# Kernel tuning notes

Hardware: AMD Instinct MI355X
Metric: run time of the kernel (lower is better)

The kernel has to match this reference:

```python
import jax, jax.numpy as jnp
import numpy as np
from jax import lax

D = 1024          # d_model
ORDER = 2         # hyena order
FILT = 64         # filter_order (implicit MLP width)
EMB = 3           # positional embedding dim (default)
INNER = D * (ORDER + 1)
DF = D * (ORDER - 1)   # filter d_model
L_MAX = 2048


def setup_inputs() -> dict:
    key = jax.random.key(0)
    ks = jax.random.split(key, 16)
    s = 0.02
    return {
        "u": jax.random.normal(ks[0], (4, L_MAX, D), jnp.float32),
        "in_w": jax.random.normal(ks[1], (D, INNER), jnp.float32) * s,
        "in_b": jnp.zeros((INNER,), jnp.float32),
        "short_w": jax.random.normal(ks[2], (INNER, 3), jnp.float32) * 0.3,
        "short_b": jnp.zeros((INNER,), jnp.float32),
        "mlp_w1": jax.random.normal(ks[3], (EMB, FILT), jnp.float32) * 0.3,
        "mlp_b1": jnp.zeros((FILT,), jnp.float32),
        "mlp_w2": jax.random.normal(ks[4], (FILT, FILT), jnp.float32) * 0.1,
        "mlp_b2": jnp.zeros((FILT,), jnp.float32),
        "mlp_w3": jax.random.normal(ks[5], (FILT, FILT), jnp.float32) * 0.1,
        "mlp_b3": jnp.zeros((FILT,), jnp.float32),
        "mlp_wo": jax.random.normal(ks[6], (FILT, DF), jnp.float32) * 0.1,
        "freq": jnp.ones((1, FILT), jnp.float32),       # shared Sin freq (w=1)
        "filt_bias": jax.random.normal(ks[7], (DF,), jnp.float32),
        "out_w": jax.random.normal(ks[8], (D, D), jnp.float32) * s,
        "out_b": jnp.zeros((D,), jnp.float32),
    }


def _pos_emb(L):
    # PositionalEmbedding(emb_dim=3): t, real/imag of exp(-i f w), bands=(3-1)//2=1
    t = jnp.linspace(0.0, 1.0, L)[:, None]                      # (L,1)
    tr = jnp.linspace(0.0, L - 1.0, L)[:, None]
    w = 2.0 * np.pi * tr / L                                    # (L,1)
    f = jnp.array([1e-4], jnp.float32)[None, :]                  # bands=1
    z = jnp.concatenate([t, jnp.cos(f * w), -jnp.sin(f * w)], axis=-1)  # (L,3)
    return z, t


def _decay(t):
    # ExponentialModulation: target=1e-2, fast=0.3, slow=1.5, shift=0
    max_d = np.log(1e-2) / 0.3
    min_d = np.log(1e-2) / 1.5
    deltas = jnp.linspace(min_d, max_d, DF)[None, :]             # (1,DF)
    return jnp.exp(-t * jnp.abs(deltas))                         # (L,DF)


def reference(u, in_w, in_b, short_w, short_b, mlp_w1, mlp_b1, mlp_w2, mlp_b2,
              mlp_w3, mlp_b3, mlp_wo, freq, filt_bias, out_w, out_b):
    B, L, _ = u.shape
    # in_proj: b l d -> b l (3d) -> b (3d) l
    up = jnp.einsum('bld,de->ble', u, in_w) + in_b
    up = up.transpose(0, 2, 1)                                   # (B, INNER, L)
    # depthwise short conv, kernel 3, padding 2 both sides, then [:L]
    uc = lax.conv_general_dilated(up, short_w[:, None, :], (1,), [(2, 2)],
                                  feature_group_count=INNER,
                                  dimension_numbers=('NCH', 'OIH', 'NCH'))
    uc = uc[..., :L] + short_b[None, :, None]
    x0, x1, v = uc[:, :D], uc[:, D:2 * D], uc[:, 2 * D:]
    # implicit long filter k(L): pos-emb -> Sin MLP (shared freq) -> modulation
    z, t = _pos_emb(L)
    h = jnp.sin(freq * (z @ mlp_w1 + mlp_b1))
    h = jnp.sin(freq * (h @ mlp_w2 + mlp_b2))
    h = jnp.sin(freq * (h @ mlp_w3 + mlp_b3))
    h = h @ mlp_wo                                               # (L, DF)
    k = (h * _decay(t)).T                                        # (DF, L) == (D, L) for order=2
    # hyena recurrence: order-1 = 1 gated fft-conv step
    vx = v * x1                                                  # (B, D, L)
    n = 2 * L
    y = jnp.fft.irfft(jnp.fft.rfft(vx, n=n) * jnp.fft.rfft(k, n=n), n=n)[..., :L]
    v = y + vx * filt_bias[None, :, None]
    # final gate + out_proj
    yv = (v * x0).transpose(0, 2, 1)                             # (B, L, D)
    return jnp.einsum('bld,de->ble', yv, out_w) + out_b
```

## Files before the change

### kernel.cpp

```cpp
#include <hip/hip_runtime.h>
#include <math.h>

#define M_PIf 3.14159265358979323846f
#define MIND (-3.0701134573253936f)
#define MAXD (-15.350567286626968f)

typedef __attribute__((ext_vector_type(8))) _Float16 f16x8;
typedef __attribute__((ext_vector_type(4))) float f32x4;
typedef __attribute__((ext_vector_type(8))) unsigned short u16x8;

#define GLDS(g, l) __builtin_amdgcn_global_load_lds(                         \
    (const __attribute__((address_space(1))) void*)(g),                      \
    (__attribute__((address_space(3))) void*)(l), 16, 0, 0)

__device__ __forceinline__ unsigned short f2h(float x) {
    return __builtin_bit_cast(unsigned short, (_Float16)x);
}
__device__ __forceinline__ float h2f(unsigned short h) {
    return (float)__builtin_bit_cast(_Float16, h);
}

__global__ __launch_bounds__(256) void prep_kernel(
    const float* __restrict__ u, unsigned short* __restrict__ uh,
    const float* __restrict__ in_w, unsigned short* __restrict__ w1t,
    const float* __restrict__ w1, const float* __restrict__ b1,
    const float* __restrict__ w2, const float* __restrict__ b2,
    const float* __restrict__ w3, const float* __restrict__ b3,
    const float* __restrict__ wo, const float* __restrict__ freq,
    float* __restrict__ kbuf)
{
    __shared__ char sm[4352];
    const int bid = blockIdx.x;
    const int tid = threadIdx.x;

    if (bid < 8192) {
        const int i = bid * 256 + tid;
        float4 v = ((const float4*)u)[i];
        ushort4 h;
        h.x = f2h(v.x); h.y = f2h(v.y); h.z = f2h(v.z); h.w = f2h(v.w);
        ((ushort4*)uh)[i] = h;
    } else if (bid < 11264) {
        float (*t)[33] = (float(*)[33])sm;
        const int idx = bid - 8192;
        const int bx = idx % 96, by = idx / 96;
        const int r0 = by * 32, c0 = bx * 32;
        const int tx = tid & 31, ty = tid >> 5;
#pragma unroll
        for (int q = 0; q < 4; ++q) {
            int r = ty + q * 8;
            t[r][tx] = in_w[(size_t)(r0 + r) * 3072 + c0 + tx];
        }
        __syncthreads();
#pragma unroll
        for (int q = 0; q < 4; ++q) {
            int cc = ty + q * 8;
            w1t[(size_t)(c0 + cc) * 1024 + r0 + tx] = f2h(t[tx][cc]);
        }
    } else {
        float (*ha)[65] = (float(*)[65])sm;
        float (*hb)[65] = (float(*)[65])(sm + 2080);
        const int l0 = (bid - 11264) * 8;
        const int uu = tid & 63, lq = tid >> 6;
#pragma unroll
        for (int p = 0; p < 2; ++p) {
            int ll = lq + p * 4;
            int l = l0 + ll;
            float t = (float)l * (1.0f / 2047.0f);
            float ang = 1e-4f * (2.0f * M_PIf) * ((float)l / 2048.0f);
            float pre = t * w1[uu] + cosf(ang) * w1[64 + uu] - sinf(ang) * w1[128 + uu] + b1[uu];
            ha[ll][uu] = sinf(freq[uu] * pre);
        }
        __syncthreads();
#pragma unroll
        for (int p = 0; p < 2; ++p) {
            int ll = lq + p * 4;
            float s = b2[uu];
#pragma unroll
            for (int i = 0; i < 64; ++i) s += ha[ll][i] * w2[i * 64 + uu];
            hb[ll][uu] = sinf(freq[uu] * s);
        }
        __syncthreads();
#pragma unroll
        for (int p = 0; p < 2; ++p) {
            int ll = lq + p * 4;
            float s = b3[uu];
#pragma unroll
            for (int i = 0; i < 64; ++i) s += hb[ll][i] * w3[i * 64 + uu];
            ha[ll][uu] = sinf(freq[uu] * s);
        }
        __syncthreads();

        float acc[4][8] = {};
        for (int i = 0; i < 64; ++i) {
            float wv[4];
#pragma unroll
            for (int q = 0; q < 4; ++q) wv[q] = wo[i * 1024 + tid + 256 * q];
#pragma unroll
            for (int l = 0; l < 8; ++l) {
                float hv = ha[l][i];
#pragma unroll
                for (int q = 0; q < 4; ++q) acc[q][l] += hv * wv[q];
            }
        }
        const float span = (MAXD - MIND) * (1.0f / 1023.0f);
#pragma unroll
        for (int q = 0; q < 4; ++q) {
            int dd = tid + 256 * q;
            float ad = fabsf(MIND + span * (float)dd);
#pragma unroll
            for (int l = 0; l < 8; ++l) {
                float t = (float)(l0 + l) * (1.0f / 2047.0f);
                kbuf[(size_t)dd * 2048 + l0 + l] = acc[q][l] * expf(-t * ad);
            }
        }
    }
}

__global__ __launch_bounds__(256) void post_kernel(
    const unsigned short* __restrict__ yvh, unsigned short* __restrict__ yvt,
    const float* __restrict__ out_w, unsigned short* __restrict__ w2t)
{
    __shared__ char sm[8448];
    const int bid = blockIdx.x;
    const int tid = threadIdx.x;
    if (bid < 2048) {
        unsigned short (*t)[66] = (unsigned short(*)[66])sm;
        const int l0 = (bid & 31) * 64;
        const int d0 = ((bid >> 5) & 15) * 64;
        const int b  = bid >> 9;
        const int rr = tid >> 4, cc = (tid & 15) * 4;
#pragma unroll
        for (int p = 0; p < 4; ++p) {
            int r = p * 16 + rr;
            ushort4 v = *(const ushort4*)&yvh[((size_t)b * 1024 + d0 + r) * 2048 + l0 + cc];
            t[cc + 0][r] = v.x; t[cc + 1][r] = v.y; t[cc + 2][r] = v.z; t[cc + 3][r] = v.w;
        }
        __syncthreads();
#pragma unroll
        for (int p = 0; p < 4; ++p) {
            int r = p * 16 + rr;
            ushort4 o;
            o.x = t[r][cc + 0]; o.y = t[r][cc + 1]; o.z = t[r][cc + 2]; o.w = t[r][cc + 3];
            *(ushort4*)&yvt[((size_t)b * 2048 + l0 + r) * 1024 + d0 + cc] = o;
        }
    } else {
        float (*t)[33] = (float(*)[33])sm;
        const int idx = bid - 2048;
        const int bx = idx & 31, by = idx >> 5;
        const int r0 = by * 32, c0 = bx * 32;
        const int tx = tid & 31, ty = tid >> 5;
#pragma unroll
        for (int q = 0; q < 4; ++q) {
            int r = ty + q * 8;
            t[r][tx] = out_w[(size_t)(r0 + r) * 1024 + c0 + tx];
        }
        __syncthreads();
#pragma unroll
        for (int q = 0; q < 4; ++q) {
            int cc = ty + q * 8;
            w2t[(size_t)(c0 + cc) * 1024 + r0 + tx] = f2h(t[tx][cc]);
        }
    }
}

template <int TRANS_OUT>
__global__ __launch_bounds__(512, 1) void gemm8_f16_kernel(
    const unsigned short* __restrict__ A, const unsigned short* __restrict__ B,
    const float* __restrict__ bias, void* __restrict__ outp)
{
    __shared__ char smem[98304];
    const int tid = threadIdx.x;
    const int wave = tid >> 6, lane = tid & 63;
    const int n0 = blockIdx.x * 128, m0 = blockIdx.y * 256;
    const int wm = wave >> 1, wn = wave & 1;
    const int rr = lane & 15, g4 = lane >> 4;
    const int srow4 = lane >> 2;
    const int sswz  = ((lane & 3) ^ ((lane >> 3) & 3)) * 8;
    const int axor  = (g4 ^ ((rr >> 1) & 3)) * 16;

    f32x4 acc[4][4] = {};
    f16x8 bq[4];

    auto stageA = [&](int bufo, int t, int kh) {
        const int ke = t * 64 + kh * 32;
        char* ldsb = smem + bufo + kh * 16384 + wave * 1024;
#pragma unroll
        for (int j = 0; j < 2; ++j) {
            const int rg = j * 128 + wave * 16 + srow4;
            GLDS((const char*)(A + (size_t)(m0 + rg) * 1024 + ke + sswz), ldsb + j * 8192);
        }
    };
    auto stageB = [&](int bufo, int t, int kh) {
        const int ke = t * 64 + kh * 32;
        const int rg = wave * 16 + srow4;
        GLDS((const char*)(B + (size_t)(n0 + rg) * 1024 + ke + sswz),
             smem + bufo + 32768 + kh * 8192 + wave * 1024);
    };

    auto phase = [&](int bufo, int s, int h, auto stage_fn, int vm) {
        const char* bb = smem + bufo;
        f16x8 aq0, aq1;
        if (h == 0) {
#pragma unroll
            for (int j = 0; j < 4; ++j)
                bq[j] = *(const f16x8*)(bb + 32768 + s * 8192 + (wn * 64 + j * 16 + rr) * 64 + axor);
        }
        aq0 = *(const f16x8*)(bb + s * 16384 + (wm * 64 + (h * 2 + 0) * 16 + rr) * 64 + axor);
        aq1 = *(const f16x8*)(bb + s * 16384 + (wm * 64 + (h * 2 + 1) * 16 + rr) * 64 + axor);
        stage_fn();
        __builtin_amdgcn_s_barrier();
        __builtin_amdgcn_s_setprio(1);
#pragma unroll
        for (int j = 0; j < 4; ++j)
            acc[h * 2 + 0][j] = __builtin_amdgcn_mfma_f32_16x16x32_f16(aq0, bq[j], acc[h * 2 + 0][j], 0, 0, 0);
#pragma unroll
        for (int j = 0; j < 4; ++j)
            acc[h * 2 + 1][j] = __builtin_amdgcn_mfma_f32_16x16x32_f16(aq1, bq[j], acc[h * 2 + 1][j], 0, 0, 0);
        __builtin_amdgcn_s_setprio(0);
        if (vm == 1) asm volatile("s_waitcnt vmcnt(3)" ::: "memory");
        else if (vm == 2) asm volatile("s_waitcnt vmcnt(0)" ::: "memory");
        __builtin_amdgcn_s_barrier();
    };

    stageA(0, 0, 0); stageB(0, 0, 0);
    stageA(0, 0, 1); stageB(0, 0, 1);
    stageA(49152, 1, 0); stageB(49152, 1, 0);
    asm volatile("s_waitcnt vmcnt(0)" ::: "memory");
    __syncthreads();

    for (int it = 0; it < 8; ++it) {
        const int T1 = 2 * it + 1, T2 = 2 * it + 2, T3 = 2 * it + 3;
        const int vmL = (it == 7) ? 2 : 1;
        phase(0,     0, 0, [&] { stageA(49152, T1, 1); }, 0);
        phase(0,     0, 1, [&] { stageB(49152, T1, 1); }, 0);
        phase(0,     1, 0, [&] { if (T2 < 16) stageA(0, T2, 0); }, 0);
        phase(0,     1, 1, [&] { if (T2 < 16) stageB(0, T2, 0); }, vmL);
        phase(49152, 0, 0, [&] { if (T2 < 16) stageA(0, T2, 1); }, 0);
        phase(49152, 0, 1, [&] { if (T2 < 16) stageB(0, T2, 1); }, 0);
        phase(49152, 1, 0, [&] { if (T3 < 16) stageA(49152, T3, 0); }, 0);
        phase(49152, 1, 1, [&] { if (T3 < 16) stageB(49152, T3, 0); }, vmL);
    }

    const int c = rr;
    if (TRANS_OUT) {
        unsigned short* up = (unsigned short*)outp;
        const int bidx = m0 >> 11;
        const int lbase = (m0 & 2047) + wm * 64 + g4 * 4;
#pragma unroll
        for (int j = 0; j < 4; ++j) {
            const int e = n0 + wn * 64 + j * 16 + c;
            const float bv = bias[e];
            unsigned short* dst = up + ((size_t)bidx * 3072 + e) * 2048 + lbase;
#pragma unroll
            for (int i = 0; i < 4; ++i) {
                ushort4 o;
                o.x = f2h(acc[i][j][0] + bv);
                o.y = f2h(acc[i][j][1] + bv);
                o.z = f2h(acc[i][j][2] + bv);
                o.w = f2h(acc[i][j][3] + bv);
                *(ushort4*)(dst + i * 16) = o;
            }
        }
    } else {
        float* op = (float*)outp;
#pragma unroll
        for (int j = 0; j < 4; ++j) {
            const int col = n0 + wn * 64 + j * 16 + c;
            const float bv = bias[col];
#pragma unroll
            for (int i = 0; i < 4; ++i) {
                const int row = m0 + wm * 64 + i * 16 + g4 * 4;
#pragma unroll
                for (int r = 0; r < 4; ++r)
                    op[(size_t)(row + r) * 1024 + col] = acc[i][j][r] + bv;
            }
        }
    }
}

__device__ __forceinline__ void conv3_chunk(
    const unsigned short* __restrict__ row, int l0,
    float wa, float wb, float wc, float sbv, float out[8])
{
    f16x8 m = *(const f16x8*)(row + l0);
    float e[10];
    if (l0 > 0) {
        ushort2 p = *(const ushort2*)(row + l0 - 2);
        e[0] = h2f(p.x); e[1] = h2f(p.y);
    } else {
        e[0] = 0.f; e[1] = 0.f;
    }
#pragma unroll
    for (int i = 0; i < 8; ++i) e[2 + i] = (float)m[i];
#pragma unroll
    for (int i = 0; i < 8; ++i)
        out[i] = wa * e[i] + wb * e[i + 1] + wc * e[i + 2] + sbv;
}

__global__ __launch_bounds__(256, 4) void conv_kernel(
    const unsigned short* __restrict__ up_t, const float* __restrict__ kbuf,
    const float* __restrict__ sw, const float* __restrict__ sb,
    const float* __restrict__ fbias, unsigned short* __restrict__ yv)
{
    __shared__ char smem[27712];
#define VH(bb) ((unsigned short*)(smem + (bb) * 4608))
#define X0(bb) ((unsigned short*)(smem + 17472 + (bb) * 5120))
    int* wpk = (int*)(smem + 9216);

    const int d = blockIdx.x;
    const int bqa = blockIdx.y * 2;
    const int tid = threadIdx.x;

    const float* kr = kbuf + (size_t)d * 2048;
    for (int xc = tid * 4; xc < 2064; xc += 1024) {
        int4 w4 = {0, 0, 0, 0};
        if (xc <= 2044) {
            const float4 fv = *(const float4*)&kr[2044 - xc];
            const float e = (xc <= 2040) ? kr[2043 - xc] : 0.f;
            w4.x = (int)((unsigned)f2h(fv.w) | ((unsigned)f2h(fv.z) << 16));
            w4.y = (int)((unsigned)f2h(fv.z) | ((unsigned)f2h(fv.y) << 16));
            w4.z = (int)((unsigned)f2h(fv.y) | ((unsigned)f2h(fv.x) << 16));
            w4.w = (int)((unsigned)f2h(fv.x) | ((unsigned)f2h(e)    << 16));
        }
        *(int4*)&wpk[xc] = w4;
    }

    const float w1a = sw[(1024 + d) * 3 + 0], w1b = sw[(1024 + d) * 3 + 1], w1c = sw[(1024 + d) * 3 + 2];
    const float w2a = sw[(2048 + d) * 3 + 0], w2b = sw[(2048 + d) * 3 + 1], w2c = sw[(2048 + d) * 3 + 2];
    const float w0a = sw[d * 3 + 0], w0b = sw[d * 3 + 1], w0c = sw[d * 3 + 2];
    const float sb1 = sb[1024 + d], sb2 = sb[2048 + d], sb0 = sb[d];
    const int l0 = tid * 8;
#pragma unroll
    for (int bb = 0; bb < 2; ++bb) {
        const int b = bqa + bb;
        const unsigned short* rx1 = up_t + ((size_t)(b * 3072) + 1024 + d) * 2048;
        const unsigned short* rv  = up_t + ((size_t)(b * 3072) + 2048 + d) * 2048;
        const unsigned short* r0  = up_t + ((size_t)(b * 3072) + d) * 2048;
        float x1v[8], vv[8], x0v[8];
        conv3_chunk(rx1, l0, w1a, w1b, w1c, sb1, x1v);
        conv3_chunk(rv,  l0, w2a, w2b, w2c, sb2, vv);
        conv3_chunk(r0,  l0, w0a, w0b, w0c, sb0, x0v);
        u16x8 o;
#pragma unroll
        for (int i = 0; i < 8; ++i) o[i] = f2h(vv[i] * x1v[i]);
        *(u16x8*)(VH(bb) + 240 + l0) = o;
        const int xo = l0 + 4 * (l0 >> 4);
        ushort4 p1, p2;
        p1.x = f2h(x0v[0]); p1.y = f2h(x0v[1]); p1.z = f2h(x0v[2]); p1.w = f2h(x0v[3]);
        p2.x = f2h(x0v[4]); p2.y = f2h(x0v[5]); p2.z = f2h(x0v[6]); p2.w = f2h(x0v[7]);
        *(ushort4*)(X0(bb) + xo) = p1;
        *(ushort4*)(X0(bb) + xo + 4) = p2;
        if (tid < 30) {
            u16x8 z = {};
            *(u16x8*)(VH(bb) + tid * 8) = z;
        }
    }
    __syncthreads();

    const int wv = tid >> 6, lane = tid & 63;
    const int row = lane & 15;
    const int sseg = lane >> 4;
    f32x4 acc[2][2] = {};
#pragma unroll
    for (int gi = 0; gi < 2; ++gi) {
        const int g = gi ? (7 - wv) : wv;
        const int tmax = 8 * g + 8;
        int xA = 2031 - row + 8 * sseg;
        int xB = 224 + 256 * g + 16 * row + 8 * sseg;
        auto step = [&]() {
            int4 avh;
            avh.x = wpk[xA];     avh.y = wpk[xA + 2];
            avh.z = wpk[xA + 4]; avh.w = wpk[xA + 6];
            f16x8 ah = __builtin_bit_cast(f16x8, avh);
#pragma unroll
            for (int bb = 0; bb < 2; ++bb) {
                f16x8 bh = *(const f16x8*)(VH(bb) + xB);
                acc[gi][bb] = __builtin_amdgcn_mfma_f32_16x16x32_f16(ah, bh, acc[gi][bb], 0, 0, 0);
            }
            xA -= 32;
            xB -= 32;
        };
        for (int t = 0; t < tmax; t += 2) { step(); step(); }
    }

    const float fb = fbias[d];
#pragma unroll
    for (int gi = 0; gi < 2; ++gi) {
        const int g = gi ? (7 - wv) : wv;
        const int lb = 256 * g + 16 * row + 4 * sseg;
#pragma unroll
        for (int bb = 0; bb < 2; ++bb) {
            ushort4 vhq = *(const ushort4*)(VH(bb) + 240 + lb);
            ushort4 x0q = *(const ushort4*)(X0(bb) + lb + 4 * (lb >> 4));
            f32x4 a = acc[gi][bb];
            ushort4 o;
            o.x = f2h((a[0] + h2f(vhq.x) * fb) * h2f(x0q.x));
            o.y = f2h((a[1] + h2f(vhq.y) * fb) * h2f(x0q.y));
            o.z = f2h((a[2] + h2f(vhq.z) * fb) * h2f(x0q.z));
            o.w = f2h((a[3] + h2f(vhq.w) * fb) * h2f(x0q.w));
            *(ushort4*)&yv[((size_t)((bqa + bb) * 1024) + d) * 2048 + lb] = o;
        }
    }
#undef VH
#undef X0
}

extern "C" void kernel_launch(void* const* d_in, const int* in_sizes, int n_in,
                              void* d_out, int out_size, void* d_ws, size_t ws_size,
                              hipStream_t stream) {
    (void)in_sizes; (void)n_in; (void)out_size; (void)ws_size;
    const float* u         = (const float*)d_in[0];
    const float* in_w      = (const float*)d_in[1];
    const float* in_b      = (const float*)d_in[2];
    const float* short_w   = (const float*)d_in[3];
    const float* short_b   = (const float*)d_in[4];
    const float* mlp_w1    = (const float*)d_in[5];
    const float* mlp_b1    = (const float*)d_in[6];
    const float* mlp_w2    = (const float*)d_in[7];
    const float* mlp_b2    = (const float*)d_in[8];
    const float* mlp_w3    = (const float*)d_in[9];
    const float* mlp_b3    = (const float*)d_in[10];
    const float* mlp_wo    = (const float*)d_in[11];
    const float* freq      = (const float*)d_in[12];
    const float* filt_bias = (const float*)d_in[13];
    const float* out_w     = (const float*)d_in[14];
    const float* out_b     = (const float*)d_in[15];
    float* out = (float*)d_out;

    char* ws = (char*)d_ws;
    const size_t MB = 1024 * 1024;
    unsigned short* up_t = (unsigned short*)ws;
    unsigned short* yvh  = (unsigned short*)(ws + 48 * MB);
    unsigned short* yvt  = (unsigned short*)(ws + 64 * MB);
    unsigned short* w2t  = (unsigned short*)(ws + 80 * MB);
    float*          kbuf = (float*)(ws + 82 * MB);
    unsigned short* uh   = (unsigned short*)(ws + 90 * MB);
    unsigned short* w1t  = (unsigned short*)(ws + 106 * MB);

    hipLaunchKernelGGL(prep_kernel, dim3(11520), dim3(256), 0, stream,
                       u, uh, in_w, w1t,
                       mlp_w1, mlp_b1, mlp_w2, mlp_b2, mlp_w3, mlp_b3, mlp_wo, freq, kbuf);
    hipLaunchKernelGGL((gemm8_f16_kernel<1>), dim3(24, 32), dim3(512), 0, stream,
                       uh, w1t, in_b, (void*)up_t);
    hipLaunchKernelGGL(conv_kernel, dim3(1024, 2), dim3(256), 0, stream,
                       up_t, kbuf, short_w, short_b, filt_bias, yvh);
    hipLaunchKernelGGL(post_kernel, dim3(3072), dim3(256), 0, stream,
                       yvh, yvt, out_w, w2t);
    hipLaunchKernelGGL((gemm8_f16_kernel<0>), dim3(8, 32), dim3(512), 0, stream,
                       yvt, w2t, out_b, (void*)out);
}
```

Measured before the change: 174.0 us.

## Restructure GEMM main loop into triple-buffered K-tiles with fewer barriers

Replaces the fine-grained eight-phase double-buffered schedule with a three-buffer ring (147 KB LDS) that prefetches two K-tiles ahead. Each iteration loads all A/B fragments for one 64-wide K tile and issues 32 MFMAs with only two barriers, instead of a barrier pair per quarter-tile. This cuts synchronization overhead and deepens the prefetch. In exchange it uses more LDS and more fragment registers, and issues whole-tile loads in bursts rather than interleaving them with compute.

```diff
diff --git a/kernel.cpp b/kernel.cpp
--- a/kernel.cpp
+++ b/kernel.cpp
@@ -168,7 +168,7 @@
     const unsigned short* __restrict__ A, const unsigned short* __restrict__ B,
     const float* __restrict__ bias, void* __restrict__ outp)
 {
-    __shared__ char smem[98304];
+    __shared__ char smem[147456];
     const int tid = threadIdx.x;
     const int wave = tid >> 6, lane = tid & 63;
     const int n0 = blockIdx.x * 128, m0 = blockIdx.y * 256;
@@ -179,7 +179,6 @@
     const int axor  = (g4 ^ ((rr >> 1) & 3)) * 16;
 
     f32x4 acc[4][4] = {};
-    f16x8 bq[4];
 
     auto stageA = [&](int bufo, int t, int kh) {
         const int ke = t * 64 + kh * 32;
@@ -196,49 +195,52 @@
         GLDS((const char*)(B + (size_t)(n0 + rg) * 1024 + ke + sswz),
              smem + bufo + 32768 + kh * 8192 + wave * 1024);
     };
-
-    auto phase = [&](int bufo, int s, int h, auto stage_fn, int vm) {
-        const char* bb = smem + bufo;
-        f16x8 aq0, aq1;
-        if (h == 0) {
-#pragma unroll
-            for (int j = 0; j < 4; ++j)
-                bq[j] = *(const f16x8*)(bb + 32768 + s * 8192 + (wn * 64 + j * 16 + rr) * 64 + axor);
-        }
-        aq0 = *(const f16x8*)(bb + s * 16384 + (wm * 64 + (h * 2 + 0) * 16 + rr) * 64 + axor);
-        aq1 = *(const f16x8*)(bb + s * 16384 + (wm * 64 + (h * 2 + 1) * 16 + rr) * 64 + axor);
-        stage_fn();
+    auto stage6 = [&](int t) {
+        const int bufo = (t % 3) * 49152;
+        stageA(bufo, t, 0); stageB(bufo, t, 0);
+        stageA(bufo, t, 1); stageB(bufo, t, 1);
+    };
+
+    stage6(0);
+    stage6(1);
+    asm volatile("s_waitcnt vmcnt(6)" ::: "memory");
+    __syncthreads();
+
+    for (int T = 0; T < 16; ++T) {
+        const char* bb = smem + (T % 3) * 49152;
+        f16x8 aq[4], bq[4];
+#pragma unroll
+        for (int j = 0; j < 4; ++j)
+            bq[j] = *(const f16x8*)(bb + 32768 + (wn * 64 + j * 16 + rr) * 64 + axor);
+#pragma unroll
+        for (int i = 0; i < 4; ++i)
+            aq[i] = *(const f16x8*)(bb + (wm * 64 + i * 16 + rr) * 64 + axor);
+        if (T + 2 < 16) stage6(T + 2);
         __builtin_amdgcn_s_barrier();
         __builtin_amdgcn_s_setprio(1);
 #pragma unroll
+        for (int i = 0; i < 4; ++i)
+#pragma unroll
+            for (int j = 0; j < 4; ++j)
+                acc[i][j] = __builtin_amdgcn_mfma_f32_16x16x32_f16(aq[i], bq[j], acc[i][j], 0, 0, 0);
+        __builtin_amdgcn_s_setprio(0);
+        f16x8 aq1[4], bq1[4];
+#pragma unroll
         for (int j = 0; j < 4; ++j)
-            acc[h * 2 + 0][j] = __builtin_amdgcn_mfma_f32_16x16x32_f16(aq0, bq[j], acc[h * 2 + 0][j], 0, 0, 0);
-#pragma unroll
-        for (int j = 0; j < 4; ++j)
-            acc[h * 2 + 1][j] = __builtin_amdgcn_mfma_f32_16x16x32_f16(aq1, bq[j], acc[h * 2 + 1][j], 0, 0, 0);
+            bq1[j] = *(const f16x8*)(bb + 32768 + 8192 + (wn * 64 + j * 16 + rr) * 64 + axor);
+#pragma unroll
+        for (int i = 0; i < 4; ++i)
+            aq1[i] = *(const f16x8*)(bb + 16384 + (wm * 64 + i * 16 + rr) * 64 + axor);
+        __builtin_amdgcn_s_setprio(1);
+#pragma unroll
+        for (int i = 0; i < 4; ++i)
+#pragma unroll
+            for (int j = 0; j < 4; ++j)
+                acc[i][j] = __builtin_amdgcn_mfma_f32_16x16x32_f16(aq1[i], bq1[j], acc[i][j], 0, 0, 0);
         __builtin_amdgcn_s_setprio(0);
-        if (vm == 1) asm volatile("s_waitcnt vmcnt(3)" ::: "memory");
-        else if (vm == 2) asm volatile("s_waitcnt vmcnt(0)" ::: "memory");
+        if (T < 14)       asm volatile("s_waitcnt vmcnt(6)" ::: "memory");
+        else if (T == 14) asm volatile("s_waitcnt vmcnt(0)" ::: "memory");
         __builtin_amdgcn_s_barrier();
-    };
-
-    stageA(0, 0, 0); stageB(0, 0, 0);
-    stageA(0, 0, 1); stageB(0, 0, 1);
-    stageA(49152, 1, 0); stageB(49152, 1, 0);
-    asm volatile("s_waitcnt vmcnt(0)" ::: "memory");
-    __syncthreads();
-
-    for (int it = 0; it < 8; ++it) {
-        const int T1 = 2 * it + 1, T2 = 2 * it + 2, T3 = 2 * it + 3;
-        const int vmL = (it == 7) ? 2 : 1;
-        phase(0,     0, 0, [&] { stageA(49152, T1, 1); }, 0);
-        phase(0,     0, 1, [&] { stageB(49152, T1, 1); }, 0);
-        phase(0,     1, 0, [&] { if (T2 < 16) stageA(0, T2, 0); }, 0);
-        phase(0,     1, 1, [&] { if (T2 < 16) stageB(0, T2, 0); }, vmL);
-        phase(49152, 0, 0, [&] { if (T2 < 16) stageA(0, T2, 1); }, 0);
-        phase(49152, 0, 1, [&] { if (T2 < 16) stageB(0, T2, 1); }, 0);
-        phase(49152, 1, 0, [&] { if (T3 < 16) stageA(49152, T3, 0); }, 0);
-        phase(49152, 1, 1, [&] { if (T3 < 16) stageB(49152, T3, 0); }, vmL);
     }
 
     const int c = rr;
```

Measured after the change: 181.5 us. 1.04x slower.
